# Kernel optimization log

Hardware: AMD Instinct MI355X
Metric: run time of the kernel (lower is better)

## Reference

```python
import jax, jax.numpy as jnp
import numpy as np
from functools import partial

B, T_OUT, T_IN, L, D_IN, D_ATT = 8, 256, 512, 128, 128, 128


def setup_inputs() -> dict:
    key = jax.random.key(0)
    ks = jax.random.split(key, 8)
    s = 0.05  # small init scale for numerical stability
    return {
        "inputs": jax.random.normal(ks[0], (B, T_OUT, D_IN), jnp.float32),
        "attended_inputs": jax.random.normal(ks[1], (B, T_IN, D_ATT), jnp.float32),
        "lstm_kernel": jax.random.normal(ks[2], (D_IN, 4 * L), jnp.float32) * s,
        "lstm_rec_kernel": jax.random.normal(ks[3], (L, 4 * L), jnp.float32) * s,
        "lstm_bias": jnp.zeros((4 * L,), jnp.float32),
        "W1": jax.random.normal(ks[4], (D_ATT, L), jnp.float32) * s,
        "b1": jnp.zeros((L,), jnp.float32),
        "W2": jax.random.normal(ks[5], (L, L), jnp.float32) * s,
        "b2": jnp.zeros((L,), jnp.float32),
        "W3": jax.random.normal(ks[6], (L, 1), jnp.float32) * s,
        "b3": jnp.zeros((1,), jnp.float32),
    }


def _lstm(x, Wk, Wr, b):
    # x: (B, T, D_in). Keras gate order: i, f, c(g), o. Zero initial state.
    Bq = x.shape[0]
    h0 = jnp.zeros((Bq, L), x.dtype)
    c0 = jnp.zeros((Bq, L), x.dtype)
    xz = jnp.einsum('btd,dk->btk', x, Wk) + b  # precompute input projection

    def step(carry, zt):
        h, c = carry
        z = zt + h @ Wr
        i, f, g, o = jnp.split(z, 4, axis=-1)
        c_new = jax.nn.sigmoid(f) * c + jax.nn.sigmoid(i) * jnp.tanh(g)
        h_new = jax.nn.sigmoid(o) * jnp.tanh(c_new)
        return (h_new, c_new), h_new

    (h_T, c_T), hs = jax.lax.scan(step, (h0, c0), jnp.swapaxes(xz, 0, 1))
    return jnp.swapaxes(hs, 0, 1), h_T, c_T  # (B, T, L), (B, L), (B, L)


def reference(inputs, attended_inputs, lstm_kernel, lstm_rec_kernel, lstm_bias,
              W1, b1, W2, b2, W3, b3):
    # setup_attended: keys = dense1(attended_inputs)
    keys = attended_inputs @ W1 + b1  # (B, T_in, L)
    x, h, c = _lstm(inputs, lstm_kernel, lstm_rec_kernel, lstm_bias)  # (B, T_out, L)
    q = x @ W2 + b2  # (B, T_out, L)
    # Bahdanau additive score: tanh(keys[:,None] + q[:,:,None]) . W3 -> (B, T_out, T_in)
    t = jnp.tanh(keys[:, None, :, :] + q[:, :, None, :])  # (B, T_out, T_in, L)
    scores = jnp.einsum('bqkl,l->bqk', t, W3[:, 0]) + b3[0]
    attn = jax.nn.softmax(scores, axis=-1)
    weighted = jnp.einsum('bqk,bkd->bqd', attn, attended_inputs)  # (B, T_out, D_att)
    out = jnp.concatenate([x, weighted], axis=2)  # (B, T_out, L + D_att)
    return out, h, c
```

## Files before the change

kernel.cpp:

```cpp
#include <hip/hip_runtime.h>
#include <hip/hip_bf16.h>

#define XF_OFF   0
#define PROG_OFF 524288
#define XZ_OFF   1048576
#define KEYS_OFF 2097152
#define OUT_H    524288
#define OUT_C    525312

#define LDS_BARRIER() __asm__ __volatile__("s_waitcnt lgkmcnt(0)\n\ts_barrier" ::: "memory")
#define PUB_BARRIER() __asm__ __volatile__("s_waitcnt vmcnt(1) lgkmcnt(0)\n\ts_barrier" ::: "memory")

#if __has_builtin(__builtin_amdgcn_exp2f)
#define EXP2F __builtin_amdgcn_exp2f
#else
#define EXP2F exp2f
#endif

typedef _Float16 f16x8 __attribute__((ext_vector_type(8)));
typedef float fx4 __attribute__((ext_vector_type(4)));

__device__ __forceinline__ float fast_rcp(float x) { return __builtin_amdgcn_rcpf(x); }
__device__ __forceinline__ float fast_sig(float v) { return fast_rcp(1.f + __expf(-v)); }
__device__ __forceinline__ float fast_tanh(float v) { return 2.f * fast_rcp(1.f + __expf(-2.f * v)) - 1.f; }

#define CSCALE (-2.8853900817779268f)

__global__ __launch_bounds__(256)
void prologue_k(const float* __restrict__ inp, const float* __restrict__ Wk,
                const float* __restrict__ bias, const float* __restrict__ att,
                const float* __restrict__ W1, const float* __restrict__ b1,
                float* __restrict__ ws) {
  __shared__ float ar[8][128];
  __shared__ float ar2[16][128];
  const int tid = threadIdx.x;

  if (blockIdx.x < 256) {
    _Float16* xz16 = (_Float16*)(ws + XZ_OFF);
    const int row0 = blockIdx.x * 8;
    for (int i = tid; i < 8 * 128; i += 256) ar[i >> 7][i & 127] = inp[row0 * 128 + i];
    __syncthreads();
    float acc[8][2];
    const float bb0 = bias[tid], bb1 = bias[tid + 256];
#pragma unroll
    for (int r = 0; r < 8; ++r) { acc[r][0] = bb0; acc[r][1] = bb1; }
    for (int d = 0; d < 128; d += 4) {
      float w0a = Wk[(d + 0) * 512 + tid], w0b = Wk[(d + 0) * 512 + tid + 256];
      float w1a = Wk[(d + 1) * 512 + tid], w1b = Wk[(d + 1) * 512 + tid + 256];
      float w2a = Wk[(d + 2) * 512 + tid], w2b = Wk[(d + 2) * 512 + tid + 256];
      float w3a = Wk[(d + 3) * 512 + tid], w3b = Wk[(d + 3) * 512 + tid + 256];
#pragma unroll
      for (int r = 0; r < 8; ++r) {
        float4 a4 = *(const float4*)&ar[r][d];
        acc[r][0] += a4.x * w0a + a4.y * w1a + a4.z * w2a + a4.w * w3a;
        acc[r][1] += a4.x * w0b + a4.y * w1b + a4.z * w2b + a4.w * w3b;
      }
    }
    const int u = tid & 127, g0 = tid >> 7;
#pragma unroll
    for (int r = 0; r < 8; ++r) {
      const int row = row0 + r, b = row >> 8, t = row & 255;
      const int base = ((t * 8 + b) * 128 + u) * 4;
      xz16[base + g0]     = (_Float16)acc[r][0];
      xz16[base + g0 + 2] = (_Float16)acc[r][1];
    }
    return;
  }

  if (blockIdx.x == 256 && tid < 2) ((int*)(ws + PROG_OFF))[tid] = 0;
  const int kb = blockIdx.x - 256;
  const int row0 = kb * 16;
  const int bq = row0 >> 9, k0 = row0 & 511;
  for (int i = tid; i < 16 * 128; i += 256) ar2[i >> 7][i & 127] = att[row0 * 128 + i];
  __syncthreads();
  const int l = tid & 127, r0 = tid >> 7;
  float acc[8];
  const float bl = b1[l];
#pragma unroll
  for (int i = 0; i < 8; ++i) acc[i] = bl;
  for (int d = 0; d < 128; d += 4) {
    float w0 = W1[(d + 0) * 128 + l], w1 = W1[(d + 1) * 128 + l];
    float w2 = W1[(d + 2) * 128 + l], w3 = W1[(d + 3) * 128 + l];
#pragma unroll
    for (int i = 0; i < 8; ++i) {
      float4 a4 = *(const float4*)&ar2[r0 * 8 + i][d];
      acc[i] += a4.x * w0 + a4.y * w1 + a4.z * w2 + a4.w * w3;
    }
  }
  float* kT = ws + KEYS_OFF + (bq * 128 + l) * 512 + k0 + r0 * 8;
  float4 lo = {acc[0], acc[1], acc[2], acc[3]};
  float4 hi = {acc[4], acc[5], acc[6], acc[7]};
  *(float4*)kT = lo;
  *(float4*)(kT + 4) = hi;
}

struct ScanS { _Float16 hb[2][576]; };
struct AttnS {
  float xr[4][128];
  float qp[4][128];
  float sc[4][512];
  float kc[8][516];
  float w3s[128];
};

__global__ __launch_bounds__(512)
void fused_scan_attn(const float* __restrict__ Wrf, const float* __restrict__ att,
                     const float* __restrict__ W2c, const float* __restrict__ b2c,
                     const float* __restrict__ W3c, const float* __restrict__ b3c,
                     float* __restrict__ ws, float* __restrict__ out) {
  __shared__ __align__(16) char smem[29312];
  const int tid = threadIdx.x;
  int* prog = (int*)(ws + PROG_OFF);
  float* xf = ws + XF_OFF;

  if (blockIdx.x == 256 || blockIdx.x == 257) return;

  if (blockIdx.x >= 2) {
    AttnS* A = (AttnS*)smem;
    const int wkr = (blockIdx.x < 256) ? (int)blockIdx.x - 2 : (int)blockIdx.x - 4;
    int cA = wkr, cB = 511 - wkr;
    if ((cA & 63) > (cB & 63)) { int tmp = cA; cA = cB; cB = tmp; }
    if (tid < 128) A->w3s[tid] = 2.f * W3c[tid];
    float sw3 = 0.f;
    for (int ll = 0; ll < 128; ll += 4) {
      float4 w4 = *(const float4*)&W3c[ll];
      sw3 += w4.x + w4.y + w4.z + w4.w;
    }
    const int l = tid & 127, r0 = tid >> 7;
    for (int ci = 0; ci < 2; ++ci) {
      const int c = ci ? cB : cA;
      const int b = c >> 6, q0 = (c & 63) * 4;
      if (tid == 0) {
        while (__hip_atomic_load(&prog[b >> 2], __ATOMIC_RELAXED, __HIP_MEMORY_SCOPE_AGENT) < q0 + 4)
          __builtin_amdgcn_s_sleep(16);
      }
      __syncthreads();
      const int row = b * 256 + q0 + r0;
      const float xv = __hip_atomic_load(&xf[row * 128 + l], __ATOMIC_RELAXED, __HIP_MEMORY_SCOPE_AGENT);
      A->xr[r0][l] = xv;
      out[row * 256 + l] = xv;
      __syncthreads();
      float qa = b2c[l];
      for (int d = 0; d < 128; d += 4) {
        float4 x4 = *(const float4*)&A->xr[r0][d];
        qa += x4.x * W2c[(d + 0) * 128 + l] + x4.y * W2c[(d + 1) * 128 + l]
            + x4.z * W2c[(d + 2) * 128 + l] + x4.w * W2c[(d + 3) * 128 + l];
      }
      A->qp[r0][l] = CSCALE * qa;
      const float base = b3c[0] - sw3;
      float acc0 = base, acc1 = base, acc2 = base, acc3 = base;
      const float* keysT = ws + KEYS_OFF + b * (128 * 512);
      for (int cc = 0; cc < 128; cc += 8) {
        __syncthreads();
        for (int i = tid; i < 8 * 512; i += 512)
          A->kc[i >> 9][i & 511] = CSCALE * keysT[(cc + (i >> 9)) * 512 + (i & 511)];
        __syncthreads();
        for (int lp = 0; lp < 8; ++lp) {
          const float qv = A->qp[r0][cc + lp];
          const float wv = A->w3s[cc + lp];
          acc0 += fast_rcp(1.f + EXP2F(A->kc[lp][l]       + qv)) * wv;
          acc1 += fast_rcp(1.f + EXP2F(A->kc[lp][l + 128] + qv)) * wv;
          acc2 += fast_rcp(1.f + EXP2F(A->kc[lp][l + 256] + qv)) * wv;
          acc3 += fast_rcp(1.f + EXP2F(A->kc[lp][l + 384] + qv)) * wv;
        }
      }
      A->sc[r0][l]       = acc0;
      A->sc[r0][l + 128] = acc1;
      A->sc[r0][l + 256] = acc2;
      A->sc[r0][l + 384] = acc3;
      __syncthreads();
      {
        const int wave = tid >> 6, lane = tid & 63;
        if (wave < 4) {
          float v[8];
#pragma unroll
          for (int i = 0; i < 8; ++i) v[i] = A->sc[wave][lane + i * 64];
          float m = v[0];
#pragma unroll
          for (int i = 1; i < 8; ++i) m = fmaxf(m, v[i]);
#pragma unroll
          for (int off = 32; off > 0; off >>= 1) m = fmaxf(m, __shfl_xor(m, off));
          float e[8], s = 0.f;
#pragma unroll
          for (int i = 0; i < 8; ++i) { e[i] = __expf(v[i] - m); s += e[i]; }
#pragma unroll
          for (int off = 32; off > 0; off >>= 1) s += __shfl_xor(s, off);
          const float inv = fast_rcp(s);
#pragma unroll
          for (int i = 0; i < 8; ++i) A->sc[wave][lane + i * 64] = e[i] * inv;
        }
      }
      __syncthreads();
      const float* attb = att + b * (512 * 128);
      float wa = 0.f;
      for (int k = 0; k < 512; k += 4) {
        float4 p4 = *(const float4*)&A->sc[r0][k];
        wa += p4.x * attb[(k + 0) * 128 + l] + p4.y * attb[(k + 1) * 128 + l]
            + p4.z * attb[(k + 2) * 128 + l] + p4.w * attb[(k + 3) * 128 + l];
      }
      out[row * 256 + 128 + l] = wa;
    }
    return;
  }

  __builtin_amdgcn_s_setprio(1);
  ScanS* S = (ScanS*)smem;
  const _Float16* xz16 = (const _Float16*)(ws + XZ_OFF);
  const int b_base = blockIdx.x * 4;
  const int w = tid >> 6, lane = tid & 63;
  const int q = lane >> 4, p = lane & 15;
  const int b = p & 3, isel = p >> 2;
  const int u = 16 * w + 4 * isel + q;
  const int bg = b_base + b;

  f16x8 afr[4][4];
#pragma unroll
  for (int i = 0; i < 4; ++i) {
    const int col = (p & 3) * 128 + 16 * w + 4 * i + (p >> 2);
#pragma unroll
    for (int kt = 0; kt < 4; ++kt)
#pragma unroll
      for (int j = 0; j < 8; ++j)
        afr[i][kt][j] = (_Float16)Wrf[(kt * 32 + q * 8 + j) * 512 + col];
  }
  {
    _Float16* hp = &S->hb[0][0];
    for (int i = tid; i < 2 * 576; i += 512) hp[i] = (_Float16)0.f;
  }
  const fx4 zeroC = {0.f, 0.f, 0.f, 0.f};
  float cst = 0.f, hval = 0.f;
  const _Float16* xp = xz16 + (bg * 128 + u) * 4;
  uint2 pf0 = *(const uint2*)(xp);
  uint2 pf1 = *(const uint2*)(xp + 4096);
  uint2 pf2 = *(const uint2*)(xp + 8192);
  __syncthreads();

  const int brow = b * 144;
  for (int t = 0; t < 256; ++t) {
    const _Float16* hrow = &S->hb[t & 1][brow];
    f16x8 bfr[4];
#pragma unroll
    for (int kt = 0; kt < 4; ++kt)
      bfr[kt] = *(const f16x8*)&hrow[kt * 32 + q * 8];
    fx4 acc[4];
#pragma unroll
    for (int i = 0; i < 4; ++i)
      acc[i] = __builtin_amdgcn_mfma_f32_16x16x32_f16(afr[i][0], bfr[0], zeroC, 0, 0, 0);
#pragma unroll
    for (int kt = 1; kt < 4; ++kt)
#pragma unroll
      for (int i = 0; i < 4; ++i)
        acc[i] = __builtin_amdgcn_mfma_f32_16x16x32_f16(afr[i][kt], bfr[kt], acc[i], 0, 0, 0);

    float z[4];
#pragma unroll
    for (int r = 0; r < 4; ++r) {
      float s01 = (isel & 1) ? acc[1][r] : acc[0][r];
      float s23 = (isel & 1) ? acc[3][r] : acc[2][r];
      z[r] = (isel & 2) ? s23 : s01;
    }

    uint2 cur = pf0;
    pf0 = pf1; pf1 = pf2;

    const _Float16* cf = (const _Float16*)&cur;
    const float zi = z[0] + (float)cf[0];
    const float zf = z[1] + (float)cf[1];
    const float zg = z[2] + (float)cf[2];
    const float zo = z[3] + (float)cf[3];
    cst = fast_sig(zf) * cst + fast_sig(zi) * fast_tanh(zg);
    hval = fast_sig(zo) * fast_tanh(cst);
    S->hb[(t + 1) & 1][brow + u] = (_Float16)hval;
    __hip_atomic_store(&xf[(bg * 256 + t) * 128 + u], hval,
                       __ATOMIC_RELAXED, __HIP_MEMORY_SCOPE_AGENT);

    if ((t & 3) == 3) {
      PUB_BARRIER();
      if (tid == 0)
        __hip_atomic_store(&prog[blockIdx.x], t,
                           __ATOMIC_RELAXED, __HIP_MEMORY_SCOPE_AGENT);
    } else {
      LDS_BARRIER();
    }
    const int t3 = (t + 3 < 256) ? t + 3 : 255;
    pf2 = *(const uint2*)(xp + t3 * 4096);
  }
  __syncthreads();
  if (tid == 0)
    __hip_atomic_store(&prog[blockIdx.x], 256,
                       __ATOMIC_RELAXED, __HIP_MEMORY_SCOPE_AGENT);
  out[OUT_H + bg * 128 + u] = hval;
  out[OUT_C + bg * 128 + u] = cst;
}

extern "C" void kernel_launch(void* const* d_in, const int* in_sizes, int n_in,
                              void* d_out, int out_size, void* d_ws, size_t ws_size,
                              hipStream_t stream) {
  const float* inputs   = (const float*)d_in[0];
  const float* attended = (const float*)d_in[1];
  const float* Wk       = (const float*)d_in[2];
  const float* Wr       = (const float*)d_in[3];
  const float* bias     = (const float*)d_in[4];
  const float* W1       = (const float*)d_in[5];
  const float* b1       = (const float*)d_in[6];
  const float* W2       = (const float*)d_in[7];
  const float* b2       = (const float*)d_in[8];
  const float* W3       = (const float*)d_in[9];
  const float* b3       = (const float*)d_in[10];
  float* out = (float*)d_out;
  float* ws = (float*)d_ws;

  hipLaunchKernelGGL(prologue_k, dim3(512), dim3(256), 0, stream,
                     inputs, Wk, bias, attended, W1, b1, ws);
  hipLaunchKernelGGL(fused_scan_attn, dim3(260), dim3(512), 0, stream,
                     Wr, attended, W2, b2, W3, b3, ws, out);
}
```

Baseline: 333.9 us.

## Double-buffer attention key tiles in LDS with register prefetch

The key tile loop now prefetches the next 8x512 key chunk into registers while computing on the current chunk, writing into a second LDS buffer. This removes one barrier per iteration and hides global load latency behind the exp/rcp compute. The CSCALE multiply moves into the keys-producing kernel, so loads are plain copies. LDS use grows to about 45 KB per block, which may reduce occupancy.

```diff
diff --git a/kernel.cpp b/kernel.cpp
--- a/kernel.cpp
+++ b/kernel.cpp
@@ -88,18 +88,18 @@
     }
   }
   float* kT = ws + KEYS_OFF + (bq * 128 + l) * 512 + k0 + r0 * 8;
-  float4 lo = {acc[0], acc[1], acc[2], acc[3]};
-  float4 hi = {acc[4], acc[5], acc[6], acc[7]};
+  float4 lo = {CSCALE * acc[0], CSCALE * acc[1], CSCALE * acc[2], CSCALE * acc[3]};
+  float4 hi = {CSCALE * acc[4], CSCALE * acc[5], CSCALE * acc[6], CSCALE * acc[7]};
   *(float4*)kT = lo;
   *(float4*)(kT + 4) = hi;
 }
 
 struct ScanS { _Float16 hb[2][576]; };
 struct AttnS {
+  float kc[2][8][512];
   float xr[4][128];
   float qp[4][128];
   float sc[4][512];
-  float kc[8][516];
   float w3s[128];
 };
 
@@ -108,7 +108,7 @@
                      const float* __restrict__ W2c, const float* __restrict__ b2c,
                      const float* __restrict__ W3c, const float* __restrict__ b3c,
                      float* __restrict__ ws, float* __restrict__ out) {
-  __shared__ __align__(16) char smem[29312];
+  __shared__ __align__(16) char smem[45568];
   const int tid = threadIdx.x;
   int* prog = (int*)(ws + PROG_OFF);
   float* xf = ws + XF_OFF;
@@ -150,19 +150,40 @@
       const float base = b3c[0] - sw3;
       float acc0 = base, acc1 = base, acc2 = base, acc3 = base;
       const float* keysT = ws + KEYS_OFF + b * (128 * 512);
+      float rg[8];
+#pragma unroll
+      for (int k = 0; k < 8; ++k) rg[k] = keysT[tid + 512 * k];
+      {
+        float* kw = &A->kc[0][0][0];
+#pragma unroll
+        for (int k = 0; k < 8; ++k) kw[tid + 512 * k] = rg[k];
+      }
+      int cur = 0;
       for (int cc = 0; cc < 128; cc += 8) {
+        const bool has_next = (cc + 8) < 128;
+        if (has_next) {
+          const float* nb = keysT + (cc + 8) * 512;
+#pragma unroll
+          for (int k = 0; k < 8; ++k) rg[k] = nb[tid + 512 * k];
+        }
         __syncthreads();
-        for (int i = tid; i < 8 * 512; i += 512)
-          A->kc[i >> 9][i & 511] = CSCALE * keysT[(cc + (i >> 9)) * 512 + (i & 511)];
-        __syncthreads();
+        const float* kb = &A->kc[cur][0][0];
+#pragma unroll
         for (int lp = 0; lp < 8; ++lp) {
           const float qv = A->qp[r0][cc + lp];
           const float wv = A->w3s[cc + lp];
-          acc0 += fast_rcp(1.f + EXP2F(A->kc[lp][l]       + qv)) * wv;
-          acc1 += fast_rcp(1.f + EXP2F(A->kc[lp][l + 128] + qv)) * wv;
-          acc2 += fast_rcp(1.f + EXP2F(A->kc[lp][l + 256] + qv)) * wv;
-          acc3 += fast_rcp(1.f + EXP2F(A->kc[lp][l + 384] + qv)) * wv;
+          const float* kr = kb + lp * 512;
+          acc0 += fast_rcp(1.f + EXP2F(kr[l]       + qv)) * wv;
+          acc1 += fast_rcp(1.f + EXP2F(kr[l + 128] + qv)) * wv;
+          acc2 += fast_rcp(1.f + EXP2F(kr[l + 256] + qv)) * wv;
+          acc3 += fast_rcp(1.f + EXP2F(kr[l + 384] + qv)) * wv;
         }
+        if (has_next) {
+          float* kw = &A->kc[cur ^ 1][0][0];
+#pragma unroll
+          for (int k = 0; k < 8; ++k) kw[tid + 512 * k] = rg[k];
+        }
+        cur ^= 1;
       }
       A->sc[r0][l]       = acc0;
       A->sc[r0][l + 128] = acc1;
```

After: 281.3 us. -15.7%, faster.
